# Kernel tuning notes

Hardware: AMD Instinct MI355X
Metric: run time of the kernel (lower is better)

## Reference

```python
import jax, jax.numpy as jnp
import numpy as np

TABLE_SIZE = 256
N_EMBD = 768
B, T = 2, 1024
VOCAB = TABLE_SIZE * TABLE_SIZE


def setup_inputs() -> dict:
    key = jax.random.key(0)
    k1, k2, k3, k4 = jax.random.split(key, 4)
    hidden_states = jax.random.normal(k1, (B, T, N_EMBD), dtype=jnp.float32)
    target_ids = jax.random.randint(k2, (B, T), 0, VOCAB, dtype=jnp.int32).astype(jnp.int64)
    W_row = jax.random.normal(k3, (TABLE_SIZE, N_EMBD), dtype=jnp.float32) * 0.02
    b_row = jnp.zeros((TABLE_SIZE,), dtype=jnp.float32)
    col_weight = jax.random.normal(k4, (TABLE_SIZE, N_EMBD, TABLE_SIZE), dtype=jnp.float32) * 0.02
    col_bias = jnp.zeros((TABLE_SIZE, TABLE_SIZE), dtype=jnp.float32)
    return {
        "hidden_states": hidden_states,
        "target_ids": target_ids,
        "W_row": W_row,
        "b_row": b_row,
        "col_weight": col_weight,
        "col_bias": col_bias,
    }


def reference(hidden_states, target_ids, W_row, b_row, col_weight, col_bias):
    table_size = col_weight.shape[0]
    # row head: (B,T,R)
    row_logits = jnp.einsum("btd,rd->btr", hidden_states, W_row) + b_row
    # codebook.lookup: factor token id over table_size x table_size grid
    row_ids = (target_ids // table_size).reshape(-1)  # (N,)
    col_ids = (target_ids % table_size).reshape(-1)   # (N,)
    hs_flat = hidden_states.reshape(-1, hidden_states.shape[-1])  # (N,d)
    # per-token hard-routed column projection (the gather + baddbmm)
    W_tok = col_weight[row_ids]                       # (N,d,C)
    col_logits = jnp.einsum("nd,ndc->nc", hs_flat, W_tok) + col_bias[row_ids]
    # cross-entropy losses (mean over tokens)
    lp_row = jax.nn.log_softmax(row_logits.reshape(-1, table_size), axis=-1)
    loss_row = -jnp.take_along_axis(lp_row, row_ids[:, None], axis=1).mean()
    lp_col = jax.nn.log_softmax(col_logits, axis=-1)
    loss_col = -jnp.take_along_axis(lp_col, col_ids[:, None], axis=1).mean()
    return loss_row + loss_col
```

## Files before the change

### kernel.cpp

```cpp
#include <hip/hip_runtime.h>
#include <math.h>

#define TABLE 256
#define DIM   768
#define CAP   512
#define NTOK_MAX 2048

__device__ __forceinline__ float4 f4zero() { return make_float4(0.f, 0.f, 0.f, 0.f); }

__global__ __launch_bounds__(256) void k_ztrans(
    const float* __restrict__ Wrow,
    float* __restrict__ WrowT,
    int* __restrict__ counts)
{
    const int d = blockIdx.x;
    const int c = threadIdx.x;
    if (d == 0) counts[c] = 0;
    WrowT[(size_t)d * TABLE + c] = Wrow[(size_t)c * DIM + d];
}

__global__ __launch_bounds__(256) void k_bucket(
    const int* __restrict__ tgt, int ntok,
    int* __restrict__ counts, int* __restrict__ bucket)
{
    const int n = blockIdx.x * 256 + threadIdx.x;
    if (n >= ntok) return;
    const int r = tgt[n] >> 8;
    const int pos = atomicAdd(&counts[r], 1);
    if (pos < CAP) bucket[r * CAP + pos] = n;
}

template<int K>
__device__ __forceinline__ void gemm_body(
    const float4* __restrict__ slab4,
    const float*  __restrict__ hs,
    const int* __restrict__ toks_s,
    int kmax,
    float (*hs_s)[DIM],
    float4 (*red)[4][32],
    const float4* __restrict__ bias4,
    int cbase,
    float* __restrict__ outp,
    int tid)
{
    const int c4 = tid & 31;
    const int dp = tid >> 5;

    for (int idx = tid; idx < K * (DIM / 4); idx += 256) {
        const int k = idx / (DIM / 4);
        const int i = idx - k * (DIM / 4);
        float4 v = f4zero();
        if (k < kmax)
            v = reinterpret_cast<const float4*>(hs + (size_t)toks_s[k] * DIM)[i];
        reinterpret_cast<float4*>(hs_s[k])[i] = v;
    }
    __syncthreads();

    float4 acc[K];
    #pragma unroll
    for (int k = 0; k < K; ++k) acc[k] = f4zero();

    const int cq = (cbase >> 2) + c4;
    #pragma unroll 4
    for (int d = dp; d < DIM; d += 8) {
        const float4 w = slab4[(size_t)d * (TABLE / 4) + cq];
        #pragma unroll
        for (int k = 0; k < K; ++k) {
            const float h = hs_s[k][d];
            acc[k].x = fmaf(h, w.x, acc[k].x);
            acc[k].y = fmaf(h, w.y, acc[k].y);
            acc[k].z = fmaf(h, w.z, acc[k].z);
            acc[k].w = fmaf(h, w.w, acc[k].w);
        }
    }

    #pragma unroll
    for (int k = 0; k < K; ++k) {
        acc[k].x += __shfl_xor(acc[k].x, 32);
        acc[k].y += __shfl_xor(acc[k].y, 32);
        acc[k].z += __shfl_xor(acc[k].z, 32);
        acc[k].w += __shfl_xor(acc[k].w, 32);
    }

    const int w    = tid >> 6;
    const int lane = tid & 63;
    constexpr int KB = (K + 3) / 4;
    for (int kb = 0; kb < KB; ++kb) {
        if (lane < 32) {
            #pragma unroll
            for (int kk = 0; kk < 4; ++kk) {
                const int k = kb * 4 + kk;
                if (k < K) red[kk][w][lane] = acc[k];
            }
        }
        __syncthreads();
        if (tid < 128) {
            const int kk = tid >> 5;
            const int cc = tid & 31;
            const int k = kb * 4 + kk;
            if (k < K && k < kmax) {
                const float4 v0 = red[kk][0][cc];
                const float4 v1 = red[kk][1][cc];
                const float4 v2 = red[kk][2][cc];
                const float4 v3 = red[kk][3][cc];
                const float4 b  = bias4[(cbase >> 2) + cc];
                float4 o;
                o.x = v0.x + v1.x + v2.x + v3.x + b.x;
                o.y = v0.y + v1.y + v2.y + v3.y + b.y;
                o.z = v0.z + v1.z + v2.z + v3.z + b.z;
                o.w = v0.w + v1.w + v2.w + v3.w + b.w;
                reinterpret_cast<float4*>(outp + (size_t)toks_s[k] * TABLE + cbase)[cc] = o;
            }
        }
        __syncthreads();
    }
}

__global__ __launch_bounds__(256) void k_gemms(
    const float* __restrict__ hs,
    const float* __restrict__ WrowT,
    const float* __restrict__ brow,
    const float* __restrict__ CW,
    const float* __restrict__ cbias,
    const int* __restrict__ counts,
    const int* __restrict__ bucket,
    float* __restrict__ row_logits,
    float* __restrict__ col_logits)
{
    __shared__ float  hs_s[16][DIM];
    __shared__ float4 red[4][4][32];
    __shared__ int    toks_s[16];

    const int bid = blockIdx.x;
    const int tid = threadIdx.x;

    if (bid < 512) {
        const int r = bid >> 1;
        const int cbase = (bid & 1) * 128;
        const int cnt = min(counts[r], CAP);
        if (cnt == 0) return;
        const float4* slab4 = reinterpret_cast<const float4*>(CW + (size_t)r * DIM * TABLE);
        const float4* bias4 = reinterpret_cast<const float4*>(cbias + (size_t)r * TABLE);
        for (int base = 0; base < cnt; base += 16) {
            const int kmax = min(16, cnt - base);
            if (tid < 16) toks_s[tid] = (tid < kmax) ? bucket[r * CAP + base + tid] : 0;
            __syncthreads();
            if (kmax <= 4)
                gemm_body<4>(slab4, hs, toks_s, kmax, hs_s, red, bias4, cbase, col_logits, tid);
            else if (kmax <= 8)
                gemm_body<8>(slab4, hs, toks_s, kmax, hs_s, red, bias4, cbase, col_logits, tid);
            else
                gemm_body<16>(slab4, hs, toks_s, kmax, hs_s, red, bias4, cbase, col_logits, tid);
        }
    } else {
        const int b = bid - 512;
        const int tile = b >> 1;
        const int cbase = (b & 1) * 128;
        if (tid < 16) toks_s[tid] = tile * 16 + tid;
        __syncthreads();
        const float4* slab4 = reinterpret_cast<const float4*>(WrowT);
        const float4* bias4 = reinterpret_cast<const float4*>(brow);
        gemm_body<16>(slab4, hs, toks_s, 16, hs_s, red, bias4, cbase, row_logits, tid);
    }
}

__device__ __forceinline__ float wave_nll(float4 v, int target, int lane) {
    float m = fmaxf(fmaxf(v.x, v.y), fmaxf(v.z, v.w));
    #pragma unroll
    for (int off = 32; off > 0; off >>= 1) m = fmaxf(m, __shfl_xor(m, off));
    float e = expf(v.x - m) + expf(v.y - m) + expf(v.z - m) + expf(v.w - m);
    float lt = 0.f;
    if (lane == (target >> 2)) {
        const int j = target & 3;
        lt = (j == 0) ? v.x : (j == 1) ? v.y : (j == 2) ? v.z : v.w;
    }
    #pragma unroll
    for (int off = 32; off > 0; off >>= 1) {
        e  += __shfl_xor(e, off);
        lt += __shfl_xor(lt, off);
    }
    return m + logf(e) - lt;
}

__global__ __launch_bounds__(256) void k_nll(
    const float* __restrict__ row_logits,
    const float* __restrict__ col_logits,
    const int* __restrict__ tgt, int ntok,
    float* __restrict__ per_tok)
{
    const int n = blockIdx.x * 4 + (threadIdx.x >> 6);
    if (n >= ntok) return;
    const int lane = threadIdx.x & 63;
    const int t = tgt[n];
    const float4 rl = reinterpret_cast<const float4*>(row_logits + (size_t)n * TABLE)[lane];
    const float4 cl = reinterpret_cast<const float4*>(col_logits + (size_t)n * TABLE)[lane];
    const float lr = wave_nll(rl, t >> 8, lane);
    const float lc = wave_nll(cl, t & 255, lane);
    if (lane == 0) per_tok[n] = lr + lc;
}

__global__ __launch_bounds__(256) void k_reduce(
    const float* __restrict__ per_tok, int ntok, float* __restrict__ out)
{
    __shared__ float red[256];
    const int c = threadIdx.x;
    float s = 0.f;
    for (int i = c; i < ntok; i += 256) s += per_tok[i];
    red[c] = s;
    __syncthreads();
    #pragma unroll
    for (int k = 128; k > 0; k >>= 1) {
        if (c < k) red[c] += red[c + k];
        __syncthreads();
    }
    if (c == 0) out[0] = red[0] / (float)ntok;
}

extern "C" void kernel_launch(void* const* d_in, const int* in_sizes, int n_in,
                              void* d_out, int out_size, void* d_ws, size_t ws_size,
                              hipStream_t stream) {
    const float* hs    = (const float*)d_in[0];
    const int*   tgt   = (const int*)d_in[1];
    const float* Wrow  = (const float*)d_in[2];
    const float* brow  = (const float*)d_in[3];
    const float* CW    = (const float*)d_in[4];
    const float* cbias = (const float*)d_in[5];
    float* out = (float*)d_out;

    const int ntok = in_sizes[1];

    char* ws = (char*)d_ws;
    int*   counts     = (int*)(ws);
    int*   bucket     = (int*)(ws + 1024);
    float* WrowT      = (float*)(ws + 1024 + 256 * CAP * 4);
    float* row_logits = (float*)((char*)WrowT + DIM * TABLE * 4);
    float* col_logits = row_logits + (size_t)ntok * TABLE;
    float* per_tok    = col_logits + (size_t)ntok * TABLE;

    k_ztrans <<<DIM, 256, 0, stream>>>(Wrow, WrowT, counts);
    k_bucket <<<(ntok + 255) / 256, 256, 0, stream>>>(tgt, ntok, counts, bucket);
    const int row_blocks = 2 * (ntok / 16);
    k_gemms  <<<512 + row_blocks, 256, 0, stream>>>(hs, WrowT, brow, CW, cbias,
                                                    counts, bucket, row_logits, col_logits);
    k_nll    <<<(ntok + 3) / 4, 256, 0, stream>>>(row_logits, col_logits, tgt, ntok, per_tok);
    k_reduce <<<1, 256, 0, stream>>>(per_tok, ntok, out);
}
```

Before: 76.29 us.

## Split column GEMM into 32-column tiles with wider D-parallel reduction

Each row slab is now split across 8 blocks of 32 columns instead of 2 blocks of 128, so four times as many blocks run. Within a block, 32 thread groups split the D dimension instead of 8, and partial sums are combined with cross-lane shuffles plus one shared-memory reduction. The K-template dispatch is removed: every tile computes 16 tokens, and empty slots are padded with a duplicate token. This aims to fill the GPU better, since only about 2048 tokens are spread over 256 rows. The cost is that each block reloads the full hidden-state tile for only 32 columns, and small buckets now do 16 tokens' worth of FMAs.

New measurement: 111.9 us. 46.7% more time.

```diff
diff --git a/kernel.cpp b/kernel.cpp
--- a/kernel.cpp
+++ b/kernel.cpp
@@ -4,7 +4,6 @@
 #define TABLE 256
 #define DIM   768
 #define CAP   512
-#define NTOK_MAX 2048
 
 __device__ __forceinline__ float4 f4zero() { return make_float4(0.f, 0.f, 0.f, 0.f); }
 
@@ -30,90 +29,86 @@
     if (pos < CAP) bucket[r * CAP + pos] = n;
 }
 
-template<int K>
-__device__ __forceinline__ void gemm_body(
+__device__ __forceinline__ void gemm_body16(
     const float4* __restrict__ slab4,
     const float*  __restrict__ hs,
     const int* __restrict__ toks_s,
     int kmax,
     float (*hs_s)[DIM],
-    float4 (*red)[4][32],
+    float4 (*red)[8][4],
     const float4* __restrict__ bias4,
     int cbase,
     float* __restrict__ outp,
     int tid)
 {
-    const int c4 = tid & 31;
-    const int dp = tid >> 5;
-
-    for (int idx = tid; idx < K * (DIM / 4); idx += 256) {
+    for (int idx = tid; idx < 16 * (DIM / 4); idx += 256) {
         const int k = idx / (DIM / 4);
         const int i = idx - k * (DIM / 4);
-        float4 v = f4zero();
-        if (k < kmax)
-            v = reinterpret_cast<const float4*>(hs + (size_t)toks_s[k] * DIM)[i];
-        reinterpret_cast<float4*>(hs_s[k])[i] = v;
-    }
-    __syncthreads();
-
-    float4 acc[K];
-    #pragma unroll
-    for (int k = 0; k < K; ++k) acc[k] = f4zero();
-
+        reinterpret_cast<float4*>(hs_s[k])[i] =
+            reinterpret_cast<const float4*>(hs + (size_t)toks_s[k] * DIM)[i];
+    }
+    __syncthreads();
+
+    const int c4 = tid & 7;
+    const int dp = tid >> 3;
     const int cq = (cbase >> 2) + c4;
-    #pragma unroll 4
-    for (int d = dp; d < DIM; d += 8) {
+
+    float4 acc[16];
+    #pragma unroll
+    for (int k = 0; k < 16; ++k) acc[k] = f4zero();
+
+    #pragma unroll 2
+    for (int d = dp; d < DIM; d += 32) {
         const float4 w = slab4[(size_t)d * (TABLE / 4) + cq];
-        #pragma unroll
-        for (int k = 0; k < K; ++k) {
-            const float h = hs_s[k][d];
-            acc[k].x = fmaf(h, w.x, acc[k].x);
-            acc[k].y = fmaf(h, w.y, acc[k].y);
-            acc[k].z = fmaf(h, w.z, acc[k].z);
-            acc[k].w = fmaf(h, w.w, acc[k].w);
-        }
-    }
-
-    #pragma unroll
-    for (int k = 0; k < K; ++k) {
-        acc[k].x += __shfl_xor(acc[k].x, 32);
-        acc[k].y += __shfl_xor(acc[k].y, 32);
-        acc[k].z += __shfl_xor(acc[k].z, 32);
-        acc[k].w += __shfl_xor(acc[k].w, 32);
-    }
-
+        float h[16];
+        #pragma unroll
+        for (int k = 0; k < 16; ++k) h[k] = hs_s[k][d];
+        #pragma unroll
+        for (int k = 0; k < 16; ++k) {
+            acc[k].x = fmaf(h[k], w.x, acc[k].x);
+            acc[k].y = fmaf(h[k], w.y, acc[k].y);
+            acc[k].z = fmaf(h[k], w.z, acc[k].z);
+            acc[k].w = fmaf(h[k], w.w, acc[k].w);
+        }
+    }
+
+    #pragma unroll
+    for (int k = 0; k < 16; ++k) {
+        #pragma unroll
+        for (int off = 8; off <= 32; off <<= 1) {
+            acc[k].x += __shfl_xor(acc[k].x, off);
+            acc[k].y += __shfl_xor(acc[k].y, off);
+            acc[k].z += __shfl_xor(acc[k].z, off);
+            acc[k].w += __shfl_xor(acc[k].w, off);
+        }
+    }
+
+    const int lane = tid & 63;
     const int w    = tid >> 6;
-    const int lane = tid & 63;
-    constexpr int KB = (K + 3) / 4;
-    for (int kb = 0; kb < KB; ++kb) {
-        if (lane < 32) {
-            #pragma unroll
-            for (int kk = 0; kk < 4; ++kk) {
-                const int k = kb * 4 + kk;
-                if (k < K) red[kk][w][lane] = acc[k];
-            }
-        }
-        __syncthreads();
-        if (tid < 128) {
-            const int kk = tid >> 5;
-            const int cc = tid & 31;
-            const int k = kb * 4 + kk;
-            if (k < K && k < kmax) {
-                const float4 v0 = red[kk][0][cc];
-                const float4 v1 = red[kk][1][cc];
-                const float4 v2 = red[kk][2][cc];
-                const float4 v3 = red[kk][3][cc];
-                const float4 b  = bias4[(cbase >> 2) + cc];
-                float4 o;
-                o.x = v0.x + v1.x + v2.x + v3.x + b.x;
-                o.y = v0.y + v1.y + v2.y + v3.y + b.y;
-                o.z = v0.z + v1.z + v2.z + v3.z + b.z;
-                o.w = v0.w + v1.w + v2.w + v3.w + b.w;
-                reinterpret_cast<float4*>(outp + (size_t)toks_s[k] * TABLE + cbase)[cc] = o;
-            }
-        }
-        __syncthreads();
-    }
+    if (lane < 8) {
+        #pragma unroll
+        for (int k = 0; k < 16; ++k) red[k][lane][w] = acc[k];
+    }
+    __syncthreads();
+
+    if (tid < 128) {
+        const int k = tid >> 3;
+        const int q = tid & 7;
+        if (k < kmax) {
+            const float4 a = red[k][q][0];
+            const float4 b = red[k][q][1];
+            const float4 c = red[k][q][2];
+            const float4 d = red[k][q][3];
+            const float4 bi = bias4[(cbase >> 2) + q];
+            float4 o;
+            o.x = a.x + b.x + c.x + d.x + bi.x;
+            o.y = a.y + b.y + c.y + d.y + bi.y;
+            o.z = a.z + b.z + c.z + d.z + bi.z;
+            o.w = a.w + b.w + c.w + d.w + bi.w;
+            reinterpret_cast<float4*>(outp + (size_t)toks_s[k] * TABLE + cbase)[q] = o;
+        }
+    }
+    __syncthreads();
 }
 
 __global__ __launch_bounds__(256) void k_gemms(
@@ -128,39 +123,36 @@
     float* __restrict__ col_logits)
 {
     __shared__ float  hs_s[16][DIM];
-    __shared__ float4 red[4][4][32];
+    __shared__ float4 red[16][8][4];
     __shared__ int    toks_s[16];
 
     const int bid = blockIdx.x;
     const int tid = threadIdx.x;
 
-    if (bid < 512) {
-        const int r = bid >> 1;
-        const int cbase = (bid & 1) * 128;
+    if (bid < 2048) {
+        const int r = bid >> 3;
+        const int cbase = (bid & 7) * 32;
         const int cnt = min(counts[r], CAP);
         if (cnt == 0) return;
         const float4* slab4 = reinterpret_cast<const float4*>(CW + (size_t)r * DIM * TABLE);
         const float4* bias4 = reinterpret_cast<const float4*>(cbias + (size_t)r * TABLE);
         for (int base = 0; base < cnt; base += 16) {
             const int kmax = min(16, cnt - base);
-            if (tid < 16) toks_s[tid] = (tid < kmax) ? bucket[r * CAP + base + tid] : 0;
+            if (tid < 16)
+                toks_s[tid] = (tid < kmax) ? bucket[r * CAP + base + tid]
+                                           : bucket[r * CAP + base];
             __syncthreads();
-            if (kmax <= 4)
-                gemm_body<4>(slab4, hs, toks_s, kmax, hs_s, red, bias4, cbase, col_logits, tid);
-            else if (kmax <= 8)
-                gemm_body<8>(slab4, hs, toks_s, kmax, hs_s, red, bias4, cbase, col_logits, tid);
-            else
-                gemm_body<16>(slab4, hs, toks_s, kmax, hs_s, red, bias4, cbase, col_logits, tid);
+            gemm_body16(slab4, hs, toks_s, kmax, hs_s, red, bias4, cbase, col_logits, tid);
         }
     } else {
-        const int b = bid - 512;
-        const int tile = b >> 1;
-        const int cbase = (b & 1) * 128;
+        const int b = bid - 2048;
+        const int tile = b >> 3;
+        const int cbase = (b & 7) * 32;
         if (tid < 16) toks_s[tid] = tile * 16 + tid;
         __syncthreads();
-        const float4* slab4 = reinterpret_cast<const float4*>(WrowT);
-        const float4* bias4 = reinterpret_cast<const float4*>(brow);
-        gemm_body<16>(slab4, hs, toks_s, 16, hs_s, red, bias4, cbase, row_logits, tid);
+        gemm_body16(reinterpret_cast<const float4*>(WrowT), hs, toks_s, 16,
+                    hs_s, red, reinterpret_cast<const float4*>(brow),
+                    cbase, row_logits, tid);
     }
 }
 
@@ -239,9 +231,9 @@
 
     k_ztrans <<<DIM, 256, 0, stream>>>(Wrow, WrowT, counts);
     k_bucket <<<(ntok + 255) / 256, 256, 0, stream>>>(tgt, ntok, counts, bucket);
-    const int row_blocks = 2 * (ntok / 16);
-    k_gemms  <<<512 + row_blocks, 256, 0, stream>>>(hs, WrowT, brow, CW, cbias,
-                                                    counts, bucket, row_logits, col_logits);
+    const int row_blocks = 8 * (ntok / 16);
+    k_gemms  <<<2048 + row_blocks, 256, 0, stream>>>(hs, WrowT, brow, CW, cbias,
+                                                     counts, bucket, row_logits, col_logits);
     k_nll    <<<(ntok + 3) / 4, 256, 0, stream>>>(row_logits, col_logits, tgt, ntok, per_tok);
     k_reduce <<<1, 256, 0, stream>>>(per_tok, ntok, out);
 }
```
